# Performance work log

Hardware: AMD Instinct MI355X
Metric: run time of the kernel (lower is better)

## Reference

```python
import jax, jax.numpy as jnp
import numpy as np

N_HOST, N_FLOW, E = 20000, 200000, 600000
D_IN, D_H, D_OUT = 64, 128, 32
NEG_SLOPE = 0.01  # F.leaky_relu default


def setup_inputs() -> dict:
    key = jax.random.key(0)
    ks = jax.random.split(key, 20)

    def w(k, shape):
        # kaiming-uniform-ish init scale (matches Linear fan-in scaling)
        lim = 1.0 / np.sqrt(shape[0])
        return jax.random.uniform(k, shape, jnp.float32, -lim, lim)

    return {
        "x_host": jax.random.normal(ks[0], (N_HOST, D_IN), jnp.float32),
        "x_flow": jax.random.normal(ks[1], (N_FLOW, D_IN), jnp.float32),
        "src_hf": jax.random.randint(ks[2], (E,), 0, N_HOST, dtype=jnp.int32),
        "dst_hf": jax.random.randint(ks[3], (E,), 0, N_FLOW, dtype=jnp.int32),
        "src_fh": jax.random.randint(ks[4], (E,), 0, N_FLOW, dtype=jnp.int32),
        "dst_fh": jax.random.randint(ks[5], (E,), 0, N_HOST, dtype=jnp.int32),
        "W0_hf_l": w(ks[6], (D_IN, D_H)), "W0_hf_r": w(ks[7], (D_IN, D_H)),
        "b0_hf": jnp.zeros((D_H,), jnp.float32),
        "W0_fh_l": w(ks[8], (D_IN, D_H)), "W0_fh_r": w(ks[9], (D_IN, D_H)),
        "b0_fh": jnp.zeros((D_H,), jnp.float32),
        "W1_hf_l": w(ks[10], (D_H, D_H)), "W1_hf_r": w(ks[11], (D_H, D_H)),
        "b1_hf": jnp.zeros((D_H,), jnp.float32),
        "W1_fh_l": w(ks[12], (D_H, D_H)), "W1_fh_r": w(ks[13], (D_H, D_H)),
        "b1_fh": jnp.zeros((D_H,), jnp.float32),
        "W_out": w(ks[14], (D_H, D_OUT)),
        "b_out": jnp.zeros((D_OUT,), jnp.float32),
    }


def _seg_mean(x, src, dst, n_dst):
    """Mean-aggregate src-node features over edges into n_dst segments."""
    s = jax.ops.segment_sum(x[src], dst, num_segments=n_dst)      # [n_dst, d]
    cnt = jax.ops.segment_sum(jnp.ones(src.shape, x.dtype), dst, num_segments=n_dst)
    return s / jnp.clip(cnt, 1.0)[:, None]


def _sage(x_src, x_dst, src, dst, Wl, Wr, b, n_dst):
    # SAGEConv: lin_l(mean_agg) + bias + lin_r(x_dst)
    agg = _seg_mean(x_src, src, dst, n_dst)
    return agg @ Wl + b + x_dst @ Wr


def reference(x_host, x_flow, src_hf, dst_hf, src_fh, dst_fh,
              W0_hf_l, W0_hf_r, b0_hf, W0_fh_l, W0_fh_r, b0_fh,
              W1_hf_l, W1_hf_r, b1_hf, W1_fh_l, W1_fh_r, b1_fh,
              W_out, b_out):
    lrelu = lambda v: jnp.where(v > 0, v, NEG_SLOPE * v)

    # layer 0
    h_flow = lrelu(_sage(x_host, x_flow, src_hf, dst_hf, W0_hf_l, W0_hf_r, b0_hf, N_FLOW))
    h_host = lrelu(_sage(x_flow, x_host, src_fh, dst_fh, W0_fh_l, W0_fh_r, b0_fh, N_HOST))

    # layer 1
    g_flow = lrelu(_sage(h_host, h_flow, src_hf, dst_hf, W1_hf_l, W1_hf_r, b1_hf, N_FLOW))
    g_host = lrelu(_sage(h_flow, h_host, src_fh, dst_fh, W1_fh_l, W1_fh_r, b1_fh, N_HOST))
    del g_host  # computed (matches module) but only 'flow' feeds the head

    return g_flow @ W_out + b_out  # [N_FLOW, D_OUT]
```

## Files before the change

### kernel.cpp

```cpp
#include <hip/hip_runtime.h>


#define N_HOST 20000
#define N_FLOW 200000
#define NEDGE  600000
#define D_IN   64
#define D_H    128
#define D_OUT  32
#define NSEG   (N_FLOW + N_HOST)
#define NBKT_F 196
#define NBKT_H 79
#define NBKT   (NBKT_F + NBKT_H)
#define NEB    586

typedef unsigned short u16;
typedef unsigned int   u32;
typedef short bf16x8 __attribute__((ext_vector_type(8)));
typedef float f32x4  __attribute__((ext_vector_type(4)));
typedef float fx2    __attribute__((ext_vector_type(2)));

__device__ __forceinline__ float bfh(u16 h) { return __uint_as_float(((u32)h) << 16); }
__device__ __forceinline__ u16 fbh(float f) {
    u32 u = __float_as_uint(f);
    return (u16)((u + 0x7fffu + ((u >> 16) & 1u)) >> 16);
}
__device__ __forceinline__ u32 packbf(float x, float y) {
    return (u32)fbh(x) | ((u32)fbh(y) << 16);
}
__device__ __forceinline__ void accp(fx2* a, uint4 u) {
    fx2 p;
    p.x = __uint_as_float(u.x << 16); p.y = __uint_as_float(u.x & 0xffff0000u); a[0] += p;
    p.x = __uint_as_float(u.y << 16); p.y = __uint_as_float(u.y & 0xffff0000u); a[1] += p;
    p.x = __uint_as_float(u.z << 16); p.y = __uint_as_float(u.z & 0xffff0000u); a[2] += p;
    p.x = __uint_as_float(u.w << 16); p.y = __uint_as_float(u.w & 0xffff0000u); a[3] += p;
}
__device__ __forceinline__ uint4 packp(const fx2* a, float inv) {
    uint4 o;
    o.x = packbf(a[0].x * inv, a[0].y * inv);
    o.y = packbf(a[1].x * inv, a[1].y * inv);
    o.z = packbf(a[2].x * inv, a[2].y * inv);
    o.w = packbf(a[3].x * inv, a[3].y * inv);
    return o;
}

template <int U>
__device__ __forceinline__ uint4 gmean(const u16* __restrict__ pool, int rs, int coff,
                                       const int* __restrict__ gcsr,
                                       const int* __restrict__ lcsr, int st0, bool fit,
                                       int st, int en) {
    fx2 a[4] = {};
    for (int e = st; e < en; e += U) {
        int n[U];
#pragma unroll
        for (int j = 0; j < U; j++)
            n[j] = (e + j < en) ? (fit ? lcsr[e + j - st0] : gcsr[e + j]) : -1;
        uint4 u[U];
#pragma unroll
        for (int j = 0; j < U; j++)
            u[j] = (n[j] >= 0) ? *(const uint4*)(pool + n[j] * rs + coff)
                               : make_uint4(0u, 0u, 0u, 0u);
#pragma unroll
        for (int j = 0; j < U; j++) accp(a, u[j]);
    }
    float inv = (en > st) ? 1.f / (float)(en - st) : 0.f;
    return packp(a, inv);
}

__global__ void k_pre(const float* __restrict__ W0_hf_l, const float* __restrict__ W0_hf_r,
                      const float* __restrict__ W0_fh_l, const float* __restrict__ W0_fh_r,
                      const float* __restrict__ W1_l, const float* __restrict__ W1_r,
                      const float* __restrict__ Wout,
                      u16* __restrict__ WT0_hf, u16* __restrict__ WT0_fh,
                      u16* __restrict__ WT1_l, u16* __restrict__ WT1_r,
                      u16* __restrict__ WTo,
                      const float* __restrict__ xf, const float* __restrict__ xh,
                      u16* __restrict__ xfb, u16* __restrict__ xhb,
                      const int* __restrict__ dst_hf, const int* __restrict__ dst_fh,
                      int* __restrict__ bcnt) {
    int b = blockIdx.x, t = threadIdx.x;
    if (b < 34) {
        u16 tmp[8];
        if (b < 32) {
            int e = (b & 7) * 2048 + t * 8;
            int n = e >> 7, k0 = e & 127;
            if (b < 8) {
#pragma unroll
                for (int j = 0; j < 8; j++) {
                    int k = k0 + j;
                    tmp[j] = fbh(k < 64 ? W0_hf_l[k * D_H + n] : W0_hf_r[(k - 64) * D_H + n]);
                }
                *(uint4*)(WT0_hf + n * 128 + k0) = *(uint4*)tmp;
            } else if (b < 16) {
#pragma unroll
                for (int j = 0; j < 8; j++) {
                    int k = k0 + j;
                    tmp[j] = fbh(k < 64 ? W0_fh_l[k * D_H + n] : W0_fh_r[(k - 64) * D_H + n]);
                }
                *(uint4*)(WT0_fh + n * 128 + k0) = *(uint4*)tmp;
            } else if (b < 24) {
#pragma unroll
                for (int j = 0; j < 8; j++) tmp[j] = fbh(W1_l[(k0 + j) * D_H + n]);
                *(uint4*)(WT1_l + n * 128 + k0) = *(uint4*)tmp;
            } else {
#pragma unroll
                for (int j = 0; j < 8; j++) tmp[j] = fbh(W1_r[(k0 + j) * D_H + n]);
                *(uint4*)(WT1_r + n * 128 + k0) = *(uint4*)tmp;
            }
        } else {
            int e = (b - 32) * 2048 + t * 8;
            int n = e >> 7, k0 = e & 127;
#pragma unroll
            for (int j = 0; j < 8; j++) tmp[j] = fbh(Wout[(k0 + j) * D_OUT + n]);
            *(uint4*)(WTo + n * 128 + k0) = *(uint4*)tmp;
        }
    } else if (b < 34 + 6875) {
        int q = (b - 34) * 256 + t;
        const int TF = (N_FLOW * D_IN) / 8;
        const int TT = TF + (N_HOST * D_IN) / 8;
        if (q >= TT) return;
        const float* src; u16* dst; int base;
        if (q < TF) { src = xf; dst = xfb; base = q * 8; }
        else        { src = xh; dst = xhb; base = (q - TF) * 8; }
        float4 f0 = *(const float4*)(src + base);
        float4 f1 = *(const float4*)(src + base + 4);
        uint4 o;
        o.x = packbf(f0.x, f0.y); o.y = packbf(f0.z, f0.w);
        o.z = packbf(f1.x, f1.y); o.w = packbf(f1.z, f1.w);
        *(uint4*)(dst + base) = o;
    } else {
        __shared__ int h[NBKT];
        for (int j = t; j < NBKT; j += 256) h[j] = 0;
        __syncthreads();
        int base = (b - 34 - 6875) * 2048;
#pragma unroll
        for (int i = 0; i < 8; i++) {
            int e = base + t + i * 256;
            if (e < 2 * NEDGE) {
                int bkt = (e < NEDGE) ? (dst_hf[e] >> 10)
                                      : (NBKT_F + (dst_fh[e - NEDGE] >> 8));
                atomicAdd(&h[bkt], 1);
            }
        }
        __syncthreads();
        for (int j = t; j < NBKT; j += 256)
            if (h[j]) atomicAdd(&bcnt[j], h[j]);
    }
}

__global__ void kb2(const int* __restrict__ src_hf, const int* __restrict__ dst_hf,
                    const int* __restrict__ src_fh, const int* __restrict__ dst_fh,
                    const int* __restrict__ bcnt, int* __restrict__ bcur,
                    int2* __restrict__ binE) {
    __shared__ int sp[512];
    __shared__ int lh[NBKT];
    __shared__ int lb[NBKT];
    int t = threadIdx.x;
    int o1 = (t < NBKT) ? bcnt[t] : 0;
    int o2 = (t + 256 < NBKT) ? bcnt[t + 256] : 0;
    sp[t] = o1; sp[t + 256] = o2;
    for (int j = t; j < NBKT; j += 256) lh[j] = 0;
    __syncthreads();
    for (int d = 1; d < 512; d <<= 1) {
        int a0 = (t >= d) ? sp[t - d] : 0;
        int a1 = sp[t + 256 - d];
        __syncthreads();
        sp[t] += a0; sp[t + 256] += a1;
        __syncthreads();
    }
    sp[t] -= o1; sp[t + 256] -= o2;
    __syncthreads();
    int base = blockIdx.x * 2048;
    int mybkt[8], myrank[8], mysrc[8], mydst[8];
#pragma unroll
    for (int i = 0; i < 8; i++) {
        int e = base + t + i * 256;
        mybkt[i] = -1;
        if (e < 2 * NEDGE) {
            int s, d;
            if (e < NEDGE) { s = src_hf[e]; d = dst_hf[e]; }
            else           { s = src_fh[e - NEDGE]; d = dst_fh[e - NEDGE] + N_FLOW; }
            int bkt = (d < N_FLOW) ? (d >> 10) : (NBKT_F + ((d - N_FLOW) >> 8));
            mybkt[i] = bkt; mysrc[i] = s; mydst[i] = d;
            myrank[i] = atomicAdd(&lh[bkt], 1);
        }
    }
    __syncthreads();
    for (int j = t; j < NBKT; j += 256)
        lb[j] = lh[j] ? atomicAdd(&bcur[j], lh[j]) : 0;
    __syncthreads();
#pragma unroll
    for (int i = 0; i < 8; i++) {
        if (mybkt[i] >= 0) {
            int pos = sp[mybkt[i]] + lb[mybkt[i]] + myrank[i];
            binE[pos] = make_int2(mysrc[i], mydst[i]);
        }
    }
}

__global__ __launch_bounds__(256) void kb3(const int2* __restrict__ binE,
                                           const int* __restrict__ bcnt,
                                           int* __restrict__ off, int* __restrict__ csr) {
    __shared__ int sp[512];
    __shared__ int deg[1024];
    __shared__ int ts[256];
    int b = blockIdx.x, t = threadIdx.x;
    sp[t] = (t < NBKT) ? bcnt[t] : 0;
    sp[t + 256] = (t + 256 < NBKT) ? bcnt[t + 256] : 0;
    __syncthreads();
    for (int d = 1; d < 512; d <<= 1) {
        int a0 = (t >= d) ? sp[t - d] : 0;
        int a1 = sp[t + 256 - d];
        __syncthreads();
        sp[t] += a0; sp[t + 256] += a1;
        __syncthreads();
    }
    int e0 = (b == 0) ? 0 : sp[b - 1];
    int e1 = sp[b];
    int nbase, ncnt;
    if (b < NBKT_F) { nbase = b << 10; ncnt = min(1024, N_FLOW - nbase); }
    else { nbase = N_FLOW + ((b - NBKT_F) << 8); ncnt = min(256, NSEG - nbase); }
    for (int i = t; i < 1024; i += 256) deg[i] = 0;
    __syncthreads();
    for (int e = e0 + t; e < e1; e += 256) {
        int2 p = binE[e];
        atomicAdd(&deg[p.y - nbase], 1);
    }
    __syncthreads();
    int loc[4]; int s = 0;
#pragma unroll
    for (int j = 0; j < 4; j++) { loc[j] = s; s += deg[t * 4 + j]; }
    ts[t] = s;
    __syncthreads();
    for (int d = 1; d < 256; d <<= 1) {
        int x = (t >= d) ? ts[t - d] : 0;
        __syncthreads();
        ts[t] += x;
        __syncthreads();
    }
    int base2 = e0 + ts[t] - s;
    int dsave[4];
#pragma unroll
    for (int j = 0; j < 4; j++) dsave[j] = deg[t * 4 + j];
    __syncthreads();
#pragma unroll
    for (int j = 0; j < 4; j++) {
        int idx = t * 4 + j;
        int st = base2 + loc[j];
        deg[idx] = st;
        if (idx < ncnt) off[nbase + idx] = st + dsave[j];
    }
    __syncthreads();
    for (int e = e0 + t; e < e1; e += 256) {
        int2 p = binE[e];
        int r = atomicAdd(&deg[p.y - nbase], 1);
        csr[r] = p.x;
    }
}

__global__ __launch_bounds__(512, 4) void k_host(
    const u16* __restrict__ xfb, const u16* __restrict__ xhb,
    const int* __restrict__ off, const int* __restrict__ csr,
    const u16* __restrict__ WT0, const float* __restrict__ b0,
    const u16* __restrict__ WT1l, u16* __restrict__ hT, int M) {
    __shared__ __align__(16) u16 sA[64 * 136];
    __shared__ int sOff[72];
    __shared__ int sCsr[2560];
    const int t = threadIdx.x;
    const int m0 = blockIdx.x * 64;
    if (t < 65) {
        int idx = N_FLOW + m0 - 1 + t;
        sOff[t] = off[min(idx, NSEG - 1)];
    }
    {
        int r = t >> 3, c = t & 7;
        int row = m0 + r;
        uint4 v = make_uint4(0u, 0u, 0u, 0u);
        if (row < M) v = *(const uint4*)(xhb + row * 64 + c * 8);
        *(uint4*)(&sA[r * 136 + 64 + c * 8]) = v;
    }
    __syncthreads();
    int st0 = sOff[0];
    int win = sOff[64] - st0;
    bool fit = (win <= 2560);
    if (fit) for (int e = t; e < win; e += 512) sCsr[e] = csr[st0 + e];
    __syncthreads();
    {
        int r = t >> 3, c = t & 7;
        int row = m0 + r;
        uint4 o = make_uint4(0u, 0u, 0u, 0u);
        if (row < M) o = gmean<8>(xfb, 64, c * 8, csr, sCsr, st0, fit, sOff[r], sOff[r + 1]);
        *(uint4*)(&sA[r * 136 + c * 8]) = o;
    }
    __syncthreads();
    const int w = t >> 6, wr = w >> 1, wc = w & 1;
    const int ln = t & 63, l15 = ln & 15, quad = ln >> 4;
    const u16* pA = sA + (wr * 16 + l15) * 136 + quad * 8;
    const u16* pB0 = WT0 + wc * 8192 + l15 * 128 + quad * 8;
    f32x4 acc[4];
#pragma unroll
    for (int tt = 0; tt < 4; tt++) acc[tt] = (f32x4){0.f, 0.f, 0.f, 0.f};
#pragma unroll
    for (int s = 0; s < 4; s++) {
        bf16x8 a = *(const bf16x8*)(pA + s * 32);
#pragma unroll
        for (int tt = 0; tt < 4; tt++) {
            bf16x8 b = *(const bf16x8*)(pB0 + tt * 2048 + s * 32);
            acc[tt] = __builtin_amdgcn_mfma_f32_16x16x32_bf16(a, b, acc[tt], 0, 0, 0);
        }
    }
    __syncthreads();
#pragma unroll
    for (int tt = 0; tt < 4; tt++) {
        int col = wc * 64 + tt * 16 + l15;
        float bv = b0[col];
#pragma unroll
        for (int i = 0; i < 4; i++) {
            int rl = wr * 16 + quad * 4 + i;
            float v = acc[tt][i] + bv;
            v = v > 0.f ? v : 0.01f * v;
            sA[rl * 136 + col] = fbh(v);
        }
    }
    __syncthreads();
    const u16* pB1 = WT1l + wc * 8192 + l15 * 128 + quad * 8;
    f32x4 accB[4];
#pragma unroll
    for (int tt = 0; tt < 4; tt++) accB[tt] = (f32x4){0.f, 0.f, 0.f, 0.f};
#pragma unroll
    for (int s = 0; s < 4; s++) {
        bf16x8 a = *(const bf16x8*)(pA + s * 32);
#pragma unroll
        for (int tt = 0; tt < 4; tt++) {
            bf16x8 b = *(const bf16x8*)(pB1 + tt * 2048 + s * 32);
            accB[tt] = __builtin_amdgcn_mfma_f32_16x16x32_bf16(a, b, accB[tt], 0, 0, 0);
        }
    }
#pragma unroll
    for (int tt = 0; tt < 4; tt++) {
        int col = wc * 64 + tt * 16 + l15;
#pragma unroll
        for (int i = 0; i < 4; i++) {
            int row = m0 + wr * 16 + quad * 4 + i;
            if (row < M) hT[row * D_H + col] = fbh(accB[tt][i]);
        }
    }
}

__global__ __launch_bounds__(512, 8) void k_mega(
    const u16* __restrict__ xfb, const u16* __restrict__ xhb,
    const int* __restrict__ off, const int* __restrict__ csr,
    const u16* __restrict__ hT,
    const u16* __restrict__ WT0, const float* __restrict__ b0,
    const u16* __restrict__ WT1r, const float* __restrict__ b1,
    const u16* __restrict__ WTo, const float* __restrict__ bout,
    float* __restrict__ OUT, int moff) {
    __shared__ __align__(16) u16 sA[64 * 136];
    __shared__ __align__(16) u16 sAg[64 * 136];
    __shared__ int sOff[72];
    __shared__ int sCsr[1024];
    const int t = threadIdx.x;
    const int m0 = (blockIdx.x + moff) * 64;
    if (t < 65) {
        int idx = m0 - 1 + t;
        sOff[t] = (idx < 0) ? 0 : off[idx];
    }
    {
        int r = t >> 3, c = t & 7;
        uint4 v = *(const uint4*)(xfb + (m0 + r) * 64 + c * 8);
        *(uint4*)(&sA[r * 136 + 64 + c * 8]) = v;
    }
    __syncthreads();
    int st0 = sOff[0];
    int win = sOff[64] - st0;
    bool fit = (win <= 1024);
    if (fit) for (int e = t; e < win; e += 512) sCsr[e] = csr[st0 + e];
    __syncthreads();
    {
        int r = t >> 3, c = t & 7;
        uint4 o = gmean<4>(xhb, 64, c * 8, csr, sCsr, st0, fit, sOff[r], sOff[r + 1]);
        *(uint4*)(&sA[r * 136 + c * 8]) = o;
    }
#pragma unroll
    for (int i = 0; i < 2; i++) {
        int q = t + i * 512;
        int r = q >> 4, c = q & 15;
        uint4 o = gmean<4>(hT, 128, c * 8, csr, sCsr, st0, fit, sOff[r], sOff[r + 1]);
        *(uint4*)(&sAg[r * 136 + c * 8]) = o;
    }
    __syncthreads();
    const int w = t >> 6, wr = w >> 1, wc = w & 1;
    const int ln = t & 63, l15 = ln & 15, quad = ln >> 4;
    const u16* pA = sA + (wr * 16 + l15) * 136 + quad * 8;
    const u16* pB0 = WT0 + wc * 8192 + l15 * 128 + quad * 8;
    f32x4 acc[4];
#pragma unroll
    for (int tt = 0; tt < 4; tt++) acc[tt] = (f32x4){0.f, 0.f, 0.f, 0.f};
#pragma unroll
    for (int s = 0; s < 4; s++) {
        bf16x8 av = *(const bf16x8*)(pA + s * 32);
#pragma unroll
        for (int tt = 0; tt < 4; tt++) {
            bf16x8 b = *(const bf16x8*)(pB0 + tt * 2048 + s * 32);
            acc[tt] = __builtin_amdgcn_mfma_f32_16x16x32_bf16(av, b, acc[tt], 0, 0, 0);
        }
    }
    __syncthreads();
#pragma unroll
    for (int tt = 0; tt < 4; tt++) {
        int col = wc * 64 + tt * 16 + l15;
        float bv = b0[col];
#pragma unroll
        for (int i = 0; i < 4; i++) {
            int rl = wr * 16 + quad * 4 + i;
            float v = acc[tt][i] + bv;
            v = v > 0.f ? v : 0.01f * v;
            sA[rl * 136 + col] = fbh(v);
        }
    }
    __syncthreads();
    const u16* pB1 = WT1r + wc * 8192 + l15 * 128 + quad * 8;
    f32x4 accB[4];
#pragma unroll
    for (int tt = 0; tt < 4; tt++) accB[tt] = (f32x4){0.f, 0.f, 0.f, 0.f};
#pragma unroll
    for (int s = 0; s < 4; s++) {
        bf16x8 av = *(const bf16x8*)(pA + s * 32);
#pragma unroll
        for (int tt = 0; tt < 4; tt++) {
            bf16x8 b = *(const bf16x8*)(pB1 + tt * 2048 + s * 32);
            accB[tt] = __builtin_amdgcn_mfma_f32_16x16x32_bf16(av, b, accB[tt], 0, 0, 0);
        }
    }
#pragma unroll
    for (int tt = 0; tt < 4; tt++) {
        int col = wc * 64 + tt * 16 + l15;
        float bv = b1[col];
#pragma unroll
        for (int i = 0; i < 4; i++) {
            int rl = wr * 16 + quad * 4 + i;
            float v = accB[tt][i] + bfh(sAg[rl * 136 + col]) + bv;
            v = v > 0.f ? v : 0.01f * v;
            sAg[rl * 136 + col] = fbh(v);
        }
    }
    __syncthreads();
    const u16* pG = sAg + (wr * 16 + l15) * 136 + quad * 8;
    const u16* pBo = WTo + wc * 2048 + l15 * 128 + quad * 8;
    f32x4 acc2 = (f32x4){0.f, 0.f, 0.f, 0.f};
#pragma unroll
    for (int s = 0; s < 4; s++) {
        bf16x8 g = *(const bf16x8*)(pG + s * 32);
        bf16x8 b = *(const bf16x8*)(pBo + s * 32);
        acc2 = __builtin_amdgcn_mfma_f32_16x16x32_bf16(g, b, acc2, 0, 0, 0);
    }
    {
        int col = wc * 16 + l15;
        float bv = bout[col];
#pragma unroll
        for (int i = 0; i < 4; i++) {
            int row = m0 + wr * 16 + quad * 4 + i;
            OUT[row * D_OUT + col] = acc2[i] + bv;
        }
    }
}

extern "C" void kernel_launch(void* const* d_in, const int* in_sizes, int n_in,
                              void* d_out, int out_size, void* d_ws, size_t ws_size,
                              hipStream_t stream) {
    const float* x_host  = (const float*)d_in[0];
    const float* x_flow  = (const float*)d_in[1];
    const int* src_hf  = (const int*)d_in[2];
    const int* dst_hf  = (const int*)d_in[3];
    const int* src_fh  = (const int*)d_in[4];
    const int* dst_fh  = (const int*)d_in[5];
    const float* W0_hf_l = (const float*)d_in[6];
    const float* W0_hf_r = (const float*)d_in[7];
    const float* b0_hf   = (const float*)d_in[8];
    const float* W0_fh_l = (const float*)d_in[9];
    const float* W0_fh_r = (const float*)d_in[10];
    const float* b0_fh   = (const float*)d_in[11];
    const float* W1_hf_l = (const float*)d_in[12];
    const float* W1_hf_r = (const float*)d_in[13];
    const float* b1_hf   = (const float*)d_in[14];
    const float* W_out   = (const float*)d_in[18];
    const float* b_out   = (const float*)d_in[19];
    float* out = (float*)d_out;

    char* ws = (char*)d_ws;
    int*  off    = (int*)(ws + 0);
    int*  csr    = (int*)(ws + 880000);
    u16*  hT     = (u16*)(ws + 5680000);
    u16*  xfb    = (u16*)(ws + 10800000);
    u16*  xhb    = (u16*)(ws + 36400000);
    int2* binE   = (int2*)(ws + 38960000);
    int*  bcnt   = (int*)(ws + 48560000);
    int*  bcur   = (int*)(ws + 48561280);
    u16*  WT0_hf = (u16*)(ws + 48562560);
    u16*  WT0_fh = (u16*)(ws + 48595328);
    u16*  WT1_l  = (u16*)(ws + 48628096);
    u16*  WT1_r  = (u16*)(ws + 48660864);
    u16*  WTo    = (u16*)(ws + 48693632);

    hipMemsetAsync(bcnt, 0, 2560, stream);
    k_pre<<<34 + 6875 + NEB, 256, 0, stream>>>(
        W0_hf_l, W0_hf_r, W0_fh_l, W0_fh_r, W1_hf_l, W1_hf_r, W_out,
        WT0_hf, WT0_fh, WT1_l, WT1_r, WTo,
        x_flow, x_host, xfb, xhb, dst_hf, dst_fh, bcnt);
    kb2<<<NEB, 256, 0, stream>>>(src_hf, dst_hf, src_fh, dst_fh, bcnt, bcur, binE);
    kb3<<<NBKT, 256, 0, stream>>>(binE, bcnt, off, csr);
    k_host<<<313, 512, 0, stream>>>(xfb, xhb, off, csr, WT0_fh, b0_fh, WT1_l, hT, N_HOST);
    k_mega<<<782, 512, 0, stream>>>(xfb, xhb, off, csr, hT, WT0_hf, b0_hf,
                                    WT1_r, b1_hf, WTo, b_out, out, 0);
    k_mega<<<782, 512, 0, stream>>>(xfb, xhb, off, csr, hT, WT0_hf, b0_hf,
                                    WT1_r, b1_hf, WTo, b_out, out, 782);
    k_mega<<<782, 512, 0, stream>>>(xfb, xhb, off, csr, hT, WT0_hf, b0_hf,
                                    WT1_r, b1_hf, WTo, b_out, out, 1564);
    k_mega<<<779, 512, 0, stream>>>(xfb, xhb, off, csr, hT, WT0_hf, b0_hf,
                                    WT1_r, b1_hf, WTo, b_out, out, 2346);
}
```

Measured before the change: 389.0 us.

## Split CSR build buckets across four blocks each and merge k_mega launches

The CSR construction kernel now launches four blocks per coarse bucket. Each block handles a quarter of the bucket's destination range: it counts edges falling below its range to find its base offset, then scans and scatters only its own sub-range. This raises parallelism from 275 blocks to 1100, at the cost of every block rereading the whole bucket's edge list. The four k_mega launches are also merged into two larger ones to cut launch overhead and tail gaps.

```diff
diff --git a/kernel.cpp b/kernel.cpp
--- a/kernel.cpp
+++ b/kernel.cpp
@@ -12,6 +12,8 @@
 #define NBKT_H 79
 #define NBKT   (NBKT_F + NBKT_H)
 #define NEB    586
+#define KB3_NF 784
+#define KB3_NH 316
 
 typedef unsigned short u16;
 typedef unsigned int   u32;
@@ -201,8 +203,9 @@
                                            const int* __restrict__ bcnt,
                                            int* __restrict__ off, int* __restrict__ csr) {
     __shared__ int sp[512];
-    __shared__ int deg[1024];
+    __shared__ int deg[256];
     __shared__ int ts[256];
+    __shared__ int below;
     int b = blockIdx.x, t = threadIdx.x;
     sp[t] = (t < NBKT) ? bcnt[t] : 0;
     sp[t + 256] = (t + 256 < NBKT) ? bcnt[t + 256] : 0;
@@ -214,22 +217,33 @@
         sp[t] += a0; sp[t + 256] += a1;
         __syncthreads();
     }
-    int e0 = (b == 0) ? 0 : sp[b - 1];
-    int e1 = sp[b];
-    int nbase, ncnt;
-    if (b < NBKT_F) { nbase = b << 10; ncnt = min(1024, N_FLOW - nbase); }
-    else { nbase = N_FLOW + ((b - NBKT_F) << 8); ncnt = min(256, NSEG - nbase); }
-    for (int i = t; i < 1024; i += 256) deg[i] = 0;
-    __syncthreads();
-    for (int e = e0 + t; e < e1; e += 256) {
+    int pbg, nbase, span, ncnt;
+    if (b < KB3_NF) {
+        pbg = b >> 2;
+        nbase = (pbg << 10) + ((b & 3) << 8);
+        span = 256;
+        ncnt = min(256, N_FLOW - nbase);
+    } else {
+        int hb = b - KB3_NF;
+        pbg = NBKT_F + (hb >> 2);
+        nbase = N_FLOW + ((hb >> 2) << 8) + ((hb & 3) << 6);
+        span = 64;
+        ncnt = min(64, NSEG - nbase);
+    }
+    int e0p = (pbg == 0) ? 0 : sp[pbg - 1];
+    int e1p = sp[pbg];
+    deg[t] = 0;
+    if (t == 0) below = 0;
+    __syncthreads();
+    for (int e = e0p + t; e < e1p; e += 256) {
         int2 p = binE[e];
-        atomicAdd(&deg[p.y - nbase], 1);
-    }
-    __syncthreads();
-    int loc[4]; int s = 0;
-#pragma unroll
-    for (int j = 0; j < 4; j++) { loc[j] = s; s += deg[t * 4 + j]; }
-    ts[t] = s;
+        int d = p.y - nbase;
+        if (d < 0) atomicAdd(&below, 1);
+        else if (d < span) atomicAdd(&deg[d], 1);
+    }
+    __syncthreads();
+    int myd = (t < span) ? deg[t] : 0;
+    ts[t] = myd;
     __syncthreads();
     for (int d = 1; d < 256; d <<= 1) {
         int x = (t >= d) ? ts[t - d] : 0;
@@ -237,23 +251,21 @@
         ts[t] += x;
         __syncthreads();
     }
-    int base2 = e0 + ts[t] - s;
-    int dsave[4];
-#pragma unroll
-    for (int j = 0; j < 4; j++) dsave[j] = deg[t * 4 + j];
-    __syncthreads();
-#pragma unroll
-    for (int j = 0; j < 4; j++) {
-        int idx = t * 4 + j;
-        int st = base2 + loc[j];
-        deg[idx] = st;
-        if (idx < ncnt) off[nbase + idx] = st + dsave[j];
-    }
-    __syncthreads();
-    for (int e = e0 + t; e < e1; e += 256) {
+    int base = e0p + below;
+    __syncthreads();
+    if (t < span) {
+        int stt = base + ts[t] - myd;
+        deg[t] = stt;
+        if (t < ncnt) off[nbase + t] = stt + myd;
+    }
+    __syncthreads();
+    for (int e = e0p + t; e < e1p; e += 256) {
         int2 p = binE[e];
-        int r = atomicAdd(&deg[p.y - nbase], 1);
-        csr[r] = p.x;
+        int d = p.y - nbase;
+        if (d >= 0 && d < span) {
+            int r = atomicAdd(&deg[d], 1);
+            csr[r] = p.x;
+        }
     }
 }
 
@@ -507,14 +519,10 @@
         WT0_hf, WT0_fh, WT1_l, WT1_r, WTo,
         x_flow, x_host, xfb, xhb, dst_hf, dst_fh, bcnt);
     kb2<<<NEB, 256, 0, stream>>>(src_hf, dst_hf, src_fh, dst_fh, bcnt, bcur, binE);
-    kb3<<<NBKT, 256, 0, stream>>>(binE, bcnt, off, csr);
+    kb3<<<KB3_NF + KB3_NH, 256, 0, stream>>>(binE, bcnt, off, csr);
     k_host<<<313, 512, 0, stream>>>(xfb, xhb, off, csr, WT0_fh, b0_fh, WT1_l, hT, N_HOST);
-    k_mega<<<782, 512, 0, stream>>>(xfb, xhb, off, csr, hT, WT0_hf, b0_hf,
-                                    WT1_r, b1_hf, WTo, b_out, out, 0);
-    k_mega<<<782, 512, 0, stream>>>(xfb, xhb, off, csr, hT, WT0_hf, b0_hf,
-                                    WT1_r, b1_hf, WTo, b_out, out, 782);
-    k_mega<<<782, 512, 0, stream>>>(xfb, xhb, off, csr, hT, WT0_hf, b0_hf,
-                                    WT1_r, b1_hf, WTo, b_out, out, 1564);
-    k_mega<<<779, 512, 0, stream>>>(xfb, xhb, off, csr, hT, WT0_hf, b0_hf,
-                                    WT1_r, b1_hf, WTo, b_out, out, 2346);
-}
+    k_mega<<<1563, 512, 0, stream>>>(xfb, xhb, off, csr, hT, WT0_hf, b0_hf,
+                                     WT1_r, b1_hf, WTo, b_out, out, 0);
+    k_mega<<<1562, 512, 0, stream>>>(xfb, xhb, off, csr, hT, WT0_hf, b0_hf,
+                                     WT1_r, b1_hf, WTo, b_out, out, 1563);
+}
```

New measurement: 369.4 us. 5.0% less time.

## Fuse x_host and h_host gathers into one edge loop and launch k_mega once

Applied to the files above, without the earlier changes.

The two separate mean-aggregation passes in k_mega (64-wide raw host features and 128-wide layer-0 host embeddings) become one loop that reads each edge's neighbor index once and issues all three vector loads together, four edges at a time. This cuts index reads and loop overhead and raises memory-level parallelism. The four chunked k_mega launches become a single 3125-block launch, and launch bounds drop to 4 waves per SIMD, which allows more registers per thread for the extra in-flight loads at some cost to occupancy.

```diff
diff --git a/kernel.cpp b/kernel.cpp
--- a/kernel.cpp
+++ b/kernel.cpp
@@ -346,20 +346,20 @@
     }
 }
 
-__global__ __launch_bounds__(512, 8) void k_mega(
+__global__ __launch_bounds__(512, 4) void k_mega(
     const u16* __restrict__ xfb, const u16* __restrict__ xhb,
     const int* __restrict__ off, const int* __restrict__ csr,
     const u16* __restrict__ hT,
     const u16* __restrict__ WT0, const float* __restrict__ b0,
     const u16* __restrict__ WT1r, const float* __restrict__ b1,
     const u16* __restrict__ WTo, const float* __restrict__ bout,
-    float* __restrict__ OUT, int moff) {
+    float* __restrict__ OUT) {
     __shared__ __align__(16) u16 sA[64 * 136];
     __shared__ __align__(16) u16 sAg[64 * 136];
     __shared__ int sOff[72];
     __shared__ int sCsr[1024];
     const int t = threadIdx.x;
-    const int m0 = (blockIdx.x + moff) * 64;
+    const int m0 = blockIdx.x * 64;
     if (t < 65) {
         int idx = m0 - 1 + t;
         sOff[t] = (idx < 0) ? 0 : off[idx];
@@ -376,16 +376,38 @@
     if (fit) for (int e = t; e < win; e += 512) sCsr[e] = csr[st0 + e];
     __syncthreads();
     {
-        int r = t >> 3, c = t & 7;
-        uint4 o = gmean<4>(xhb, 64, c * 8, csr, sCsr, st0, fit, sOff[r], sOff[r + 1]);
-        *(uint4*)(&sA[r * 136 + c * 8]) = o;
-    }
-#pragma unroll
-    for (int i = 0; i < 2; i++) {
-        int q = t + i * 512;
-        int r = q >> 4, c = q & 15;
-        uint4 o = gmean<4>(hT, 128, c * 8, csr, sCsr, st0, fit, sOff[r], sOff[r + 1]);
-        *(uint4*)(&sAg[r * 136 + c * 8]) = o;
+        const int r = t >> 3, c = t & 7;
+        const int st = sOff[r], en = sOff[r + 1];
+        fx2 a0[4] = {}, a1[4] = {}, a2[4] = {};
+        for (int e = st; e < en; e += 4) {
+            int n[4];
+#pragma unroll
+            for (int j = 0; j < 4; j++)
+                n[j] = (e + j < en) ? (fit ? sCsr[e + j - st0] : csr[e + j]) : -1;
+            uint4 ux[4], ua[4], ub[4];
+#pragma unroll
+            for (int j = 0; j < 4; j++) {
+                if (n[j] >= 0) {
+                    const u16* px = xhb + n[j] * 64 + c * 8;
+                    const u16* ph = hT + n[j] * 128 + c * 16;
+                    ux[j] = *(const uint4*)px;
+                    ua[j] = *(const uint4*)ph;
+                    ub[j] = *(const uint4*)(ph + 8);
+                } else {
+                    ux[j] = make_uint4(0u, 0u, 0u, 0u);
+                    ua[j] = make_uint4(0u, 0u, 0u, 0u);
+                    ub[j] = make_uint4(0u, 0u, 0u, 0u);
+                }
+            }
+#pragma unroll
+            for (int j = 0; j < 4; j++) {
+                accp(a0, ux[j]); accp(a1, ua[j]); accp(a2, ub[j]);
+            }
+        }
+        float inv = (en > st) ? 1.f / (float)(en - st) : 0.f;
+        *(uint4*)(&sA[r * 136 + c * 8]) = packp(a0, inv);
+        *(uint4*)(&sAg[r * 136 + c * 16]) = packp(a1, inv);
+        *(uint4*)(&sAg[r * 136 + c * 16 + 8]) = packp(a2, inv);
     }
     __syncthreads();
     const int w = t >> 6, wr = w >> 1, wc = w & 1;
@@ -509,12 +531,6 @@
     kb2<<<NEB, 256, 0, stream>>>(src_hf, dst_hf, src_fh, dst_fh, bcnt, bcur, binE);
     kb3<<<NBKT, 256, 0, stream>>>(binE, bcnt, off, csr);
     k_host<<<313, 512, 0, stream>>>(xfb, xhb, off, csr, WT0_fh, b0_fh, WT1_l, hT, N_HOST);
-    k_mega<<<782, 512, 0, stream>>>(xfb, xhb, off, csr, hT, WT0_hf, b0_hf,
-                                    WT1_r, b1_hf, WTo, b_out, out, 0);
-    k_mega<<<782, 512, 0, stream>>>(xfb, xhb, off, csr, hT, WT0_hf, b0_hf,
-                                    WT1_r, b1_hf, WTo, b_out, out, 782);
-    k_mega<<<782, 512, 0, stream>>>(xfb, xhb, off, csr, hT, WT0_hf, b0_hf,
-                                    WT1_r, b1_hf, WTo, b_out, out, 1564);
-    k_mega<<<779, 512, 0, stream>>>(xfb, xhb, off, csr, hT, WT0_hf, b0_hf,
-                                    WT1_r, b1_hf, WTo, b_out, out, 2346);
-}
+    k_mega<<<3125, 512, 0, stream>>>(xfb, xhb, off, csr, hT, WT0_hf, b0_hf,
+                                     WT1_r, b1_hf, WTo, b_out, out);
+}
```

Result: faster. 352.6 us (-9.4%).
